# Kernel tuning notes

Hardware: AMD Instinct MI355X
Metric: run time of the kernel (lower is better)

## Reference

```python
import jax, jax.numpy as jnp
import numpy as np

B, N, D = 256, 64, 128
E, K, T = 8, 2, 80
H = 2 * D  # expert hidden


def setup_inputs() -> dict:
    key = jax.random.key(0)
    ks = jax.random.split(key, 4)
    s = 1.0 / np.sqrt(D)
    return {
        "x": jax.random.normal(ks[0], (B, N, D), dtype=jnp.float32),
        "router_w": jax.random.normal(ks[1], (D, E), dtype=jnp.float32) * s,
        "router_b": jnp.zeros((E,), dtype=jnp.float32),
        "w1": jax.random.normal(ks[2], (E, D, H), dtype=jnp.float32) * s,
        "b1": jnp.zeros((E, H), dtype=jnp.float32),
        "w2": jax.random.normal(ks[3], (E, H, T * 2), dtype=jnp.float32) * (1.0 / np.sqrt(H)),
        "b2": jnp.zeros((E, T * 2), dtype=jnp.float32),
        "A": N,
    }


def reference(x, router_w, router_b, w1, b1, w2, b2, A):
    k = K
    xa = x[:, 1:A]                                   # [B, A-1, D] agents w/o ego
    # --- router: per-sample logits -> softmax -> top-k gates ---
    pooled = xa.mean(axis=1)                         # [B, D]
    logits = pooled @ router_w + router_b            # [B, E]
    probs = jax.nn.softmax(logits, axis=-1)
    topk_probs, topk_idx = jax.lax.top_k(probs, k)   # [B, k]
    # dense gate matrix: sum_k p_k * onehot(idx_k)
    gates = jnp.sum(jax.nn.one_hot(topk_idx, E, dtype=probs.dtype)
                    * topk_probs[..., None], axis=1)  # [B, E]
    # --- experts: per-agent MLP, all experts batched (grouped GEMM form) ---
    h = jax.nn.relu(jnp.einsum('bnd,edh->ebnh', xa, w1) + b1[:, None, None, :])
    out_e = jnp.einsum('ebnh,eho->ebno', h, w2) + b2[:, None, None, :]  # [E,B,A-1,T*2]
    out_e = out_e.reshape(E, out_e.shape[1], out_e.shape[2], T, 2)
    # --- weighted combine (scatter-combine expressed densely) ---
    output = jnp.einsum('be,ebntc->bntc', gates, out_e)  # [B, A-1, T, 2]
    return output
```

## Files before the change

### kernel.cpp

```cpp
#include <hip/hip_runtime.h>
#include <hip/hip_bf16.h>

#define B_   256
#define N_   64
#define D_   128
#define E_   8
#define T_   80
#define H_   256
#define O_   160
#define NTOK 63

typedef __bf16 bf16x8 __attribute__((ext_vector_type(8)));
typedef float  f32x4  __attribute__((ext_vector_type(4)));
typedef unsigned short u16x8 __attribute__((ext_vector_type(8)));
typedef unsigned short u16x4 __attribute__((ext_vector_type(4)));

struct Route { int e0, e1; float g0, g1; };

__device__ __forceinline__ unsigned short f2bf(float f) {
    unsigned int u = __builtin_bit_cast(unsigned int, f);
    u += 0x7FFFu + ((u >> 16) & 1u);
    return (unsigned short)(u >> 16);
}

__global__ void prep_w(const float* __restrict__ w1, const float* __restrict__ w2,
                       unsigned short* __restrict__ w1t, unsigned short* __restrict__ w2t) {
    int idx = blockIdx.x * 256 + threadIdx.x;
    if (idx < E_ * H_ * D_) {
        int d = idx & (D_ - 1);
        int h = (idx >> 7) & (H_ - 1);
        int e = idx >> 15;
        w1t[idx] = f2bf(w1[((size_t)e * D_ + d) * H_ + h]);
    }
    if (idx < E_ * O_ * H_) {
        int h = idx & (H_ - 1);
        int rest = idx >> 8;
        int o = rest % O_;
        int e = rest / O_;
        w2t[idx] = f2bf(w2[((size_t)e * H_ + h) * O_ + o]);
    }
}

__global__ void router_kernel(const float* __restrict__ x,
                              const float* __restrict__ rw,
                              const float* __restrict__ rb,
                              Route* __restrict__ rt) {
    int b = blockIdx.x;
    int lane = threadIdx.x;
    __shared__ float pooled[D_];
    __shared__ float logits[E_];
    float s0 = 0.f, s1 = 0.f;
    const float* xb = x + (size_t)b * N_ * D_;
    for (int n = 1; n < N_; ++n) {
        s0 += xb[n * D_ + lane];
        s1 += xb[n * D_ + lane + 64];
    }
    pooled[lane]      = s0 * (1.f / 63.f);
    pooled[lane + 64] = s1 * (1.f / 63.f);
    __syncthreads();
    if (lane < E_) {
        float acc = rb[lane];
        for (int d = 0; d < D_; ++d) acc += pooled[d] * rw[d * E_ + lane];
        logits[lane] = acc;
    }
    __syncthreads();
    if (lane == 0) {
        float mx = logits[0];
        for (int e = 1; e < E_; ++e) mx = fmaxf(mx, logits[e]);
        float p[E_]; float den = 0.f;
        for (int e = 0; e < E_; ++e) { p[e] = expf(logits[e] - mx); den += p[e]; }
        float inv = 1.f / den;
        for (int e = 0; e < E_; ++e) p[e] *= inv;
        int i0 = 0;
        for (int e = 1; e < E_; ++e) if (p[e] > p[i0]) i0 = e;
        int i1 = (i0 == 0) ? 1 : 0;
        for (int e = 0; e < E_; ++e) if (e != i0 && p[e] > p[i1]) i1 = e;
        Route r; r.e0 = i0; r.e1 = i1; r.g0 = p[i0]; r.g1 = p[i1];
        rt[b] = r;
    }
}

__global__ __launch_bounds__(256)
void moe_main(const float* __restrict__ x,
              const float* __restrict__ b1,
              const float* __restrict__ b2,
              const unsigned short* __restrict__ w1t,
              const unsigned short* __restrict__ w2t,
              const Route* __restrict__ rt,
              float* __restrict__ out) {
    const int half = blockIdx.x;
    const int b    = blockIdx.y;
    const int m0   = half * 32;
    const int t    = threadIdx.x;
    const int wv   = t >> 6;
    const int lane = t & 63;
    const int q    = lane >> 4;
    const int r16  = lane & 15;

    __shared__ unsigned short xa_lds[32 * 128];
    __shared__ unsigned short h_lds[32 * 256];

    {
        int row  = t >> 3;
        int col0 = (t & 7) * 16;
        int n = m0 + row;
        bool valid = (n < NTOK);
        const float* src = x + ((size_t)b * N_ + (1 + n)) * D_ + col0;
        #pragma unroll
        for (int c = 0; c < 4; ++c) {
            float4 v;
            if (valid) v = *(const float4*)(src + c * 4);
            else       v = make_float4(0.f, 0.f, 0.f, 0.f);
            u16x4 h4;
            h4[0] = f2bf(v.x); h4[1] = f2bf(v.y); h4[2] = f2bf(v.z); h4[3] = f2bf(v.w);
            int col = col0 + c * 4;
            *(u16x4*)&xa_lds[row * 128 + (col ^ ((row & 7) << 3))] = h4;
        }
    }

    Route rr = rt[b];
    const f32x4 z4 = {0.f, 0.f, 0.f, 0.f};
    f32x4 acc2[2][3];
    #pragma unroll
    for (int mt = 0; mt < 2; ++mt)
        #pragma unroll
        for (int j = 0; j < 3; ++j) acc2[mt][j] = z4;

    __syncthreads();

    #pragma unroll
    for (int s = 0; s < 2; ++s) {
        const int   e = s ? rr.e1 : rr.e0;
        const float g = s ? rr.g1 : rr.g0;
        const unsigned short* w1e = w1t + (size_t)e * H_ * D_;

        f32x4 acc1[2][4];
        #pragma unroll
        for (int mt = 0; mt < 2; ++mt)
            #pragma unroll
            for (int nt = 0; nt < 4; ++nt) acc1[mt][nt] = z4;

        #pragma unroll
        for (int ks = 0; ks < 4; ++ks) {
            int col0 = ks * 32 + q * 8;
            int row0 = r16, row1 = 16 + r16;
            bf16x8 a0 = __builtin_bit_cast(bf16x8,
                *(const u16x8*)&xa_lds[row0 * 128 + (col0 ^ ((row0 & 7) << 3))]);
            bf16x8 a1 = __builtin_bit_cast(bf16x8,
                *(const u16x8*)&xa_lds[row1 * 128 + (col0 ^ ((row1 & 7) << 3))]);
            #pragma unroll
            for (int nt = 0; nt < 4; ++nt) {
                int col = wv * 64 + nt * 16 + r16;
                bf16x8 bb = __builtin_bit_cast(bf16x8,
                    *(const u16x8*)(w1e + (size_t)col * D_ + ks * 32 + q * 8));
                acc1[0][nt] = __builtin_amdgcn_mfma_f32_16x16x32_bf16(a0, bb, acc1[0][nt], 0, 0, 0);
                acc1[1][nt] = __builtin_amdgcn_mfma_f32_16x16x32_bf16(a1, bb, acc1[1][nt], 0, 0, 0);
            }
        }

        if (s == 1) __syncthreads();

        float b1v[4];
        #pragma unroll
        for (int nt = 0; nt < 4; ++nt) b1v[nt] = b1[e * H_ + wv * 64 + nt * 16 + r16];
        #pragma unroll
        for (int mt = 0; mt < 2; ++mt)
            #pragma unroll
            for (int nt = 0; nt < 4; ++nt) {
                int col = wv * 64 + nt * 16 + r16;
                #pragma unroll
                for (int rg = 0; rg < 4; ++rg) {
                    int row = mt * 16 + q * 4 + rg;
                    float v = acc1[mt][nt][rg] + b1v[nt];
                    v = fmaxf(v, 0.f) * g;
                    h_lds[row * 256 + (col ^ ((row & 7) << 3))] = f2bf(v);
                }
            }
        __syncthreads();

        const unsigned short* w2e = w2t + (size_t)e * O_ * H_;
        #pragma unroll
        for (int ks = 0; ks < 8; ++ks) {
            int col0 = ks * 32 + q * 8;
            int row0 = r16, row1 = 16 + r16;
            bf16x8 a0 = __builtin_bit_cast(bf16x8,
                *(const u16x8*)&h_lds[row0 * 256 + (col0 ^ ((row0 & 7) << 3))]);
            bf16x8 a1 = __builtin_bit_cast(bf16x8,
                *(const u16x8*)&h_lds[row1 * 256 + (col0 ^ ((row1 & 7) << 3))]);
            #pragma unroll
            for (int j = 0; j < 3; ++j) {
                int nt2 = wv + j * 4;
                if (nt2 < 10) {
                    int col = nt2 * 16 + r16;
                    bf16x8 bb = __builtin_bit_cast(bf16x8,
                        *(const u16x8*)(w2e + (size_t)col * H_ + col0));
                    acc2[0][j] = __builtin_amdgcn_mfma_f32_16x16x32_bf16(a0, bb, acc2[0][j], 0, 0, 0);
                    acc2[1][j] = __builtin_amdgcn_mfma_f32_16x16x32_bf16(a1, bb, acc2[1][j], 0, 0, 0);
                }
            }
        }
    }

    #pragma unroll
    for (int j = 0; j < 3; ++j) {
        int nt2 = wv + j * 4;
        if (nt2 < 10) {
            int col = nt2 * 16 + r16;
            float bias = rr.g0 * b2[rr.e0 * O_ + col] + rr.g1 * b2[rr.e1 * O_ + col];
            #pragma unroll
            for (int mt = 0; mt < 2; ++mt)
                #pragma unroll
                for (int rg = 0; rg < 4; ++rg) {
                    int row = mt * 16 + q * 4 + rg;
                    int n = m0 + row;
                    if (n < NTOK)
                        out[((size_t)b * NTOK + n) * O_ + col] = acc2[mt][j][rg] + bias;
                }
        }
    }
}

extern "C" void kernel_launch(void* const* d_in, const int* in_sizes, int n_in,
                              void* d_out, int out_size, void* d_ws, size_t ws_size,
                              hipStream_t stream) {
    const float* x  = (const float*)d_in[0];
    const float* rw = (const float*)d_in[1];
    const float* rb = (const float*)d_in[2];
    const float* w1 = (const float*)d_in[3];
    const float* b1 = (const float*)d_in[4];
    const float* w2 = (const float*)d_in[5];
    const float* b2 = (const float*)d_in[6];
    float* out = (float*)d_out;

    unsigned short* w1t = (unsigned short*)d_ws;
    unsigned short* w2t = w1t + (size_t)E_ * H_ * D_;
    Route* rt = (Route*)(w2t + (size_t)E_ * O_ * H_);

    prep_w<<<1280, 256, 0, stream>>>(w1, w2, w1t, w2t);
    router_kernel<<<B_, 64, 0, stream>>>(x, rw, rb, rt);
    moe_main<<<dim3(2, B_), 256, 0, stream>>>(x, b1, b2, w1t, w2t, rt, out);
}
```

Measured before the change: 110.4 us.

## Fuse router into MoE kernel and tile-transpose weight prep via LDS

Moves the router (mean pooling, logits, softmax, top-2) into the main MoE kernel, reusing the x tile already loaded for the expert GEMM. This drops a kernel launch and a second read of x. Each block now covers all 64 tokens of a sample with 512 threads, so expert weights are fetched once per sample instead of twice. The weight prep kernel now transposes 32x32 tiles through shared memory to get coalesced reads and writes. The trade-off is half as many blocks (256), which lowers parallelism, plus extra block-level syncs before the GEMMs start.

```diff
diff --git a/kernel.cpp b/kernel.cpp
--- a/kernel.cpp
+++ b/kernel.cpp
@@ -15,110 +15,133 @@
 typedef unsigned short u16x8 __attribute__((ext_vector_type(8)));
 typedef unsigned short u16x4 __attribute__((ext_vector_type(4)));
 
-struct Route { int e0, e1; float g0, g1; };
-
 __device__ __forceinline__ unsigned short f2bf(float f) {
     unsigned int u = __builtin_bit_cast(unsigned int, f);
     u += 0x7FFFu + ((u >> 16) & 1u);
     return (unsigned short)(u >> 16);
 }
 
-__global__ void prep_w(const float* __restrict__ w1, const float* __restrict__ w2,
-                       unsigned short* __restrict__ w1t, unsigned short* __restrict__ w2t) {
-    int idx = blockIdx.x * 256 + threadIdx.x;
-    if (idx < E_ * H_ * D_) {
-        int d = idx & (D_ - 1);
-        int h = (idx >> 7) & (H_ - 1);
-        int e = idx >> 15;
-        w1t[idx] = f2bf(w1[((size_t)e * D_ + d) * H_ + h]);
-    }
-    if (idx < E_ * O_ * H_) {
-        int h = idx & (H_ - 1);
-        int rest = idx >> 8;
-        int o = rest % O_;
-        int e = rest / O_;
-        w2t[idx] = f2bf(w2[((size_t)e * H_ + h) * O_ + o]);
-    }
-}
-
-__global__ void router_kernel(const float* __restrict__ x,
-                              const float* __restrict__ rw,
-                              const float* __restrict__ rb,
-                              Route* __restrict__ rt) {
-    int b = blockIdx.x;
-    int lane = threadIdx.x;
-    __shared__ float pooled[D_];
-    __shared__ float logits[E_];
-    float s0 = 0.f, s1 = 0.f;
-    const float* xb = x + (size_t)b * N_ * D_;
-    for (int n = 1; n < N_; ++n) {
-        s0 += xb[n * D_ + lane];
-        s1 += xb[n * D_ + lane + 64];
-    }
-    pooled[lane]      = s0 * (1.f / 63.f);
-    pooled[lane + 64] = s1 * (1.f / 63.f);
-    __syncthreads();
-    if (lane < E_) {
-        float acc = rb[lane];
-        for (int d = 0; d < D_; ++d) acc += pooled[d] * rw[d * E_ + lane];
-        logits[lane] = acc;
-    }
-    __syncthreads();
-    if (lane == 0) {
-        float mx = logits[0];
-        for (int e = 1; e < E_; ++e) mx = fmaxf(mx, logits[e]);
-        float p[E_]; float den = 0.f;
-        for (int e = 0; e < E_; ++e) { p[e] = expf(logits[e] - mx); den += p[e]; }
-        float inv = 1.f / den;
-        for (int e = 0; e < E_; ++e) p[e] *= inv;
-        int i0 = 0;
-        for (int e = 1; e < E_; ++e) if (p[e] > p[i0]) i0 = e;
-        int i1 = (i0 == 0) ? 1 : 0;
-        for (int e = 0; e < E_; ++e) if (e != i0 && p[e] > p[i1]) i1 = e;
-        Route r; r.e0 = i0; r.e1 = i1; r.g0 = p[i0]; r.g1 = p[i1];
-        rt[b] = r;
-    }
-}
-
 __global__ __launch_bounds__(256)
-void moe_main(const float* __restrict__ x,
-              const float* __restrict__ b1,
-              const float* __restrict__ b2,
-              const unsigned short* __restrict__ w1t,
-              const unsigned short* __restrict__ w2t,
-              const Route* __restrict__ rt,
-              float* __restrict__ out) {
-    const int half = blockIdx.x;
-    const int b    = blockIdx.y;
-    const int m0   = half * 32;
+void prep_w(const float* __restrict__ w1, const float* __restrict__ w2,
+            unsigned short* __restrict__ w1t, unsigned short* __restrict__ w2t) {
+    __shared__ float tile[32][33];
+    const int bid = blockIdx.x;
+    const int t = threadIdx.x;
+    const int r  = t >> 3;
+    const int c4 = (t & 7) * 4;
+
+    const float* src; unsigned short* dst;
+    int src_ld, dst_ld;
+    size_t soff, doff;
+    if (bid < 256) {
+        int e = bid >> 5, rest = bid & 31;
+        int dt = rest >> 3, ht = rest & 7;
+        soff = ((size_t)e * 128 + dt * 32) * 256 + ht * 32; src_ld = 256;
+        doff = ((size_t)e * 256 + ht * 32) * 128 + dt * 32; dst_ld = 128;
+        src = w1; dst = w1t;
+    } else {
+        int id = bid - 256;
+        int e = id / 40, rest = id % 40;
+        int ht = rest / 5, ot = rest % 5;
+        soff = ((size_t)e * 256 + ht * 32) * 160 + ot * 32; src_ld = 160;
+        doff = ((size_t)e * 160 + ot * 32) * 256 + ht * 32; dst_ld = 256;
+        src = w2; dst = w2t;
+    }
+    float4 v = *(const float4*)(src + soff + (size_t)r * src_ld + c4);
+    tile[r][c4 + 0] = v.x; tile[r][c4 + 1] = v.y;
+    tile[r][c4 + 2] = v.z; tile[r][c4 + 3] = v.w;
+    __syncthreads();
+    const int c  = t >> 3;
+    const int r4 = (t & 7) * 4;
+    u16x4 h4;
+    h4[0] = f2bf(tile[r4 + 0][c]); h4[1] = f2bf(tile[r4 + 1][c]);
+    h4[2] = f2bf(tile[r4 + 2][c]); h4[3] = f2bf(tile[r4 + 3][c]);
+    *(u16x4*)(dst + doff + (size_t)c * dst_ld + r4) = h4;
+}
+
+__global__ __launch_bounds__(512)
+void moe_fused(const float* __restrict__ x,
+               const float* __restrict__ rw,
+               const float* __restrict__ rb,
+               const float* __restrict__ b1,
+               const float* __restrict__ b2,
+               const unsigned short* __restrict__ w1t,
+               const unsigned short* __restrict__ w2t,
+               float* __restrict__ out) {
+    const int b    = blockIdx.x;
     const int t    = threadIdx.x;
     const int wv   = t >> 6;
     const int lane = t & 63;
+    const int wvM  = wv >> 2;
+    const int wvN  = wv & 3;
     const int q    = lane >> 4;
     const int r16  = lane & 15;
 
-    __shared__ unsigned short xa_lds[32 * 128];
-    __shared__ unsigned short h_lds[32 * 256];
+    __shared__ unsigned short xa_lds[64 * 128];
+    __shared__ unsigned short h_lds[64 * 256];
+    __shared__ float part[16][128];
+    __shared__ float pooled[128];
+    __shared__ int   re_s[2];
+    __shared__ float rg_s[2];
 
     {
-        int row  = t >> 3;
-        int col0 = (t & 7) * 16;
-        int n = m0 + row;
-        bool valid = (n < NTOK);
-        const float* src = x + ((size_t)b * N_ + (1 + n)) * D_ + col0;
-        #pragma unroll
-        for (int c = 0; c < 4; ++c) {
-            float4 v;
-            if (valid) v = *(const float4*)(src + c * 4);
-            else       v = make_float4(0.f, 0.f, 0.f, 0.f);
+        const int rbase = t >> 5;
+        const int c0    = (t & 31) * 4;
+        float4 ps = make_float4(0.f, 0.f, 0.f, 0.f);
+        const float* xb = x + ((size_t)b * N_ + 1) * D_;
+        #pragma unroll
+        for (int rr = 0; rr < 4; ++rr) {
+            int row = rbase + rr * 16;
+            float4 v = make_float4(0.f, 0.f, 0.f, 0.f);
+            if (row < NTOK) v = *(const float4*)(xb + (size_t)row * D_ + c0);
+            ps.x += v.x; ps.y += v.y; ps.z += v.z; ps.w += v.w;
             u16x4 h4;
-            h4[0] = f2bf(v.x); h4[1] = f2bf(v.y); h4[2] = f2bf(v.z); h4[3] = f2bf(v.w);
-            int col = col0 + c * 4;
-            *(u16x4*)&xa_lds[row * 128 + (col ^ ((row & 7) << 3))] = h4;
-        }
-    }
-
-    Route rr = rt[b];
+            h4[0] = f2bf(v.x); h4[1] = f2bf(v.y);
+            h4[2] = f2bf(v.z); h4[3] = f2bf(v.w);
+            *(u16x4*)&xa_lds[row * 128 + (c0 ^ ((row & 7) << 3))] = h4;
+        }
+        *(float4*)&part[rbase][c0] = ps;
+    }
+    __syncthreads();
+
+    if (t < 128) {
+        float s = 0.f;
+        #pragma unroll
+        for (int i = 0; i < 16; ++i) s += part[i][t];
+        pooled[t] = s * (1.f / 63.f);
+    }
+    __syncthreads();
+
+    if (t < 64) {
+        int e  = lane >> 3;
+        int dg = lane & 7;
+        float p = 0.f;
+        #pragma unroll
+        for (int i = 0; i < 16; ++i)
+            p += pooled[dg * 16 + i] * rw[(dg * 16 + i) * E_ + e];
+        p += __shfl_xor(p, 1); p += __shfl_xor(p, 2); p += __shfl_xor(p, 4);
+        float lg[E_];
+        #pragma unroll
+        for (int e2 = 0; e2 < E_; ++e2) lg[e2] = __shfl(p, e2 * 8) + rb[e2];
+        if (lane == 0) {
+            float mx = lg[0];
+            for (int i = 1; i < E_; ++i) mx = fmaxf(mx, lg[i]);
+            float pr[E_]; float den = 0.f;
+            for (int i = 0; i < E_; ++i) { pr[i] = expf(lg[i] - mx); den += pr[i]; }
+            int i0 = 0;
+            for (int i = 1; i < E_; ++i) if (pr[i] > pr[i0]) i0 = i;
+            int i1 = (i0 == 0) ? 1 : 0;
+            for (int i = 0; i < E_; ++i) if (i != i0 && pr[i] > pr[i1]) i1 = i;
+            float inv = 1.f / den;
+            re_s[0] = i0; re_s[1] = i1;
+            rg_s[0] = pr[i0] * inv; rg_s[1] = pr[i1] * inv;
+        }
+    }
+    __syncthreads();
+
+    const int   e0 = re_s[0], e1 = re_s[1];
+    const float g0 = rg_s[0], g1 = rg_s[1];
+
     const f32x4 z4 = {0.f, 0.f, 0.f, 0.f};
     f32x4 acc2[2][3];
     #pragma unroll
@@ -126,12 +149,10 @@
         #pragma unroll
         for (int j = 0; j < 3; ++j) acc2[mt][j] = z4;
 
-    __syncthreads();
-
     #pragma unroll
     for (int s = 0; s < 2; ++s) {
-        const int   e = s ? rr.e1 : rr.e0;
-        const float g = s ? rr.g1 : rr.g0;
+        const int   e = s ? e1 : e0;
+        const float g = s ? g1 : g0;
         const unsigned short* w1e = w1t + (size_t)e * H_ * D_;
 
         f32x4 acc1[2][4];
@@ -140,19 +161,20 @@
             #pragma unroll
             for (int nt = 0; nt < 4; ++nt) acc1[mt][nt] = z4;
 
+        const int row0 = wvM * 32 + r16;
+        const int row1 = wvM * 32 + 16 + r16;
         #pragma unroll
         for (int ks = 0; ks < 4; ++ks) {
-            int col0 = ks * 32 + q * 8;
-            int row0 = r16, row1 = 16 + r16;
+            int col0k = ks * 32 + q * 8;
             bf16x8 a0 = __builtin_bit_cast(bf16x8,
-                *(const u16x8*)&xa_lds[row0 * 128 + (col0 ^ ((row0 & 7) << 3))]);
+                *(const u16x8*)&xa_lds[row0 * 128 + (col0k ^ ((row0 & 7) << 3))]);
             bf16x8 a1 = __builtin_bit_cast(bf16x8,
-                *(const u16x8*)&xa_lds[row1 * 128 + (col0 ^ ((row1 & 7) << 3))]);
+                *(const u16x8*)&xa_lds[row1 * 128 + (col0k ^ ((row1 & 7) << 3))]);
             #pragma unroll
             for (int nt = 0; nt < 4; ++nt) {
-                int col = wv * 64 + nt * 16 + r16;
+                int col = wvN * 64 + nt * 16 + r16;
                 bf16x8 bb = __builtin_bit_cast(bf16x8,
-                    *(const u16x8*)(w1e + (size_t)col * D_ + ks * 32 + q * 8));
+                    *(const u16x8*)(w1e + (size_t)col * D_ + col0k));
                 acc1[0][nt] = __builtin_amdgcn_mfma_f32_16x16x32_bf16(a0, bb, acc1[0][nt], 0, 0, 0);
                 acc1[1][nt] = __builtin_amdgcn_mfma_f32_16x16x32_bf16(a1, bb, acc1[1][nt], 0, 0, 0);
             }
@@ -162,15 +184,15 @@
 
         float b1v[4];
         #pragma unroll
-        for (int nt = 0; nt < 4; ++nt) b1v[nt] = b1[e * H_ + wv * 64 + nt * 16 + r16];
+        for (int nt = 0; nt < 4; ++nt) b1v[nt] = b1[e * H_ + wvN * 64 + nt * 16 + r16];
         #pragma unroll
         for (int mt = 0; mt < 2; ++mt)
             #pragma unroll
             for (int nt = 0; nt < 4; ++nt) {
-                int col = wv * 64 + nt * 16 + r16;
+                int col = wvN * 64 + nt * 16 + r16;
                 #pragma unroll
                 for (int rg = 0; rg < 4; ++rg) {
-                    int row = mt * 16 + q * 4 + rg;
+                    int row = wvM * 32 + mt * 16 + q * 4 + rg;
                     float v = acc1[mt][nt][rg] + b1v[nt];
                     v = fmaxf(v, 0.f) * g;
                     h_lds[row * 256 + (col ^ ((row & 7) << 3))] = f2bf(v);
@@ -181,19 +203,18 @@
         const unsigned short* w2e = w2t + (size_t)e * O_ * H_;
         #pragma unroll
         for (int ks = 0; ks < 8; ++ks) {
-            int col0 = ks * 32 + q * 8;
-            int row0 = r16, row1 = 16 + r16;
+            int col0k = ks * 32 + q * 8;
             bf16x8 a0 = __builtin_bit_cast(bf16x8,
-                *(const u16x8*)&h_lds[row0 * 256 + (col0 ^ ((row0 & 7) << 3))]);
+                *(const u16x8*)&h_lds[row0 * 256 + (col0k ^ ((row0 & 7) << 3))]);
             bf16x8 a1 = __builtin_bit_cast(bf16x8,
-                *(const u16x8*)&h_lds[row1 * 256 + (col0 ^ ((row1 & 7) << 3))]);
+                *(const u16x8*)&h_lds[row1 * 256 + (col0k ^ ((row1 & 7) << 3))]);
             #pragma unroll
             for (int j = 0; j < 3; ++j) {
-                int nt2 = wv + j * 4;
+                int nt2 = wvN + j * 4;
                 if (nt2 < 10) {
                     int col = nt2 * 16 + r16;
                     bf16x8 bb = __builtin_bit_cast(bf16x8,
-                        *(const u16x8*)(w2e + (size_t)col * H_ + col0));
+                        *(const u16x8*)(w2e + (size_t)col * H_ + col0k));
                     acc2[0][j] = __builtin_amdgcn_mfma_f32_16x16x32_bf16(a0, bb, acc2[0][j], 0, 0, 0);
                     acc2[1][j] = __builtin_amdgcn_mfma_f32_16x16x32_bf16(a1, bb, acc2[1][j], 0, 0, 0);
                 }
@@ -203,16 +224,15 @@
 
     #pragma unroll
     for (int j = 0; j < 3; ++j) {
-        int nt2 = wv + j * 4;
+        int nt2 = wvN + j * 4;
         if (nt2 < 10) {
             int col = nt2 * 16 + r16;
-            float bias = rr.g0 * b2[rr.e0 * O_ + col] + rr.g1 * b2[rr.e1 * O_ + col];
+            float bias = g0 * b2[e0 * O_ + col] + g1 * b2[e1 * O_ + col];
             #pragma unroll
             for (int mt = 0; mt < 2; ++mt)
                 #pragma unroll
                 for (int rg = 0; rg < 4; ++rg) {
-                    int row = mt * 16 + q * 4 + rg;
-                    int n = m0 + row;
+                    int n = wvM * 32 + mt * 16 + q * 4 + rg;
                     if (n < NTOK)
                         out[((size_t)b * NTOK + n) * O_ + col] = acc2[mt][j][rg] + bias;
                 }
@@ -234,9 +254,7 @@
 
     unsigned short* w1t = (unsigned short*)d_ws;
     unsigned short* w2t = w1t + (size_t)E_ * H_ * D_;
-    Route* rt = (Route*)(w2t + (size_t)E_ * O_ * H_);
-
-    prep_w<<<1280, 256, 0, stream>>>(w1, w2, w1t, w2t);
-    router_kernel<<<B_, 64, 0, stream>>>(x, rw, rb, rt);
-    moe_main<<<dim3(2, B_), 256, 0, stream>>>(x, b1, b2, w1t, w2t, rt, out);
-}
+
+    prep_w<<<576, 256, 0, stream>>>(w1, w2, w1t, w2t);
+    moe_fused<<<B_, 512, 0, stream>>>(x, rw, rb, b1, b2, w1t, w2t, out);
+}
```

Result: faster. 99.34 us (-10.0%).
